# Optimization experiments

Measured on AMD Instinct MI355X. Metric: run time of the kernel, lower is better.

## Reference

```python
import jax, jax.numpy as jnp
import numpy as np

B, T, D, H, E = 2, 1024, 1024, 4096, 8


def setup_inputs() -> dict:
    key = jax.random.key(0)
    ks = jax.random.split(key, 6)
    x = jax.random.normal(ks[0], (B, T, D), dtype=jnp.float32)
    padding_mask = jnp.zeros((B, T), dtype=bool)
    # Gate: Linear(D, E, bias=False) -> weight (E, D)
    Wg = jax.random.normal(ks[1], (E, D), dtype=jnp.float32) * (1.0 / np.sqrt(D))
    # Stacked expert FFN params (torch Linear layout: weight (out, in))
    W1 = jax.random.normal(ks[2], (E, H, D), dtype=jnp.float32) * (1.0 / np.sqrt(D))
    b1 = jax.random.normal(ks[3], (E, H), dtype=jnp.float32) * 0.01
    W2 = jax.random.normal(ks[4], (E, D, H), dtype=jnp.float32) * (1.0 / np.sqrt(H))
    b2 = jax.random.normal(ks[5], (E, D), dtype=jnp.float32) * 0.01
    return {"x": x, "padding_mask": padding_mask, "Wg": Wg, "W1": W1, "b1": b1, "W2": W2, "b2": b2}


def _top2_gate(xt, pm, Wg):
    # xt: (nt, D) flattened tokens, pm: (nt,) bool padding mask
    nt, ec = xt.shape[0], Wg.shape[0]
    logits = (xt @ Wg.T).astype(jnp.float32)            # use_fp32=True
    gate_value = jax.nn.softmax(logits, axis=-1)        # (nt, E)
    gate_value = jnp.where(pm[:, None], 0.0, gate_value)
    top2_idx = jax.lax.top_k(gate_value, 2)[1]          # (nt, 2)
    keep = jax.nn.one_hot(top2_idx, ec, dtype=bool).any(axis=1)  # (nt, E) True at top1/top2
    gate_weights = jnp.where(keep, gate_value, 0.0)
    s = gate_weights.sum(axis=1, keepdims=True)
    s = jnp.where(s == 0.0, 1.0, s)
    gate_weights = gate_weights / s
    # load-balance loss: fraction of top-1 assignments vs mean gate prob per expert
    nt_real = (~pm).sum().astype(jnp.float32)
    top1_counts = (jax.nn.one_hot(top2_idx[:, 0], ec, dtype=jnp.float32)
                   * (~pm)[:, None].astype(jnp.float32)).sum(axis=0)  # (E,)
    lb_loss = ec * ((top1_counts / nt_real) * (gate_value.sum(axis=0) / nt_real)).sum()
    return lb_loss, gate_weights, gate_value


def reference(x, padding_mask, Wg, W1, b1, W2, b2):
    Bx, Tx, Dx = x.shape
    xt = x.reshape(-1, Dx)                   # (nt, D)
    pm = padding_mask.reshape(-1)            # (nt,)
    lb_loss, gw, gate_value = _top2_gate(xt, pm, Wg)
    gw = gw.astype(x.dtype)                  # (nt, E)
    # Expert FFNs (dense over experts; routing weights are zero except top-2)
    h = jax.nn.relu(jnp.einsum('nd,ehd->neh', xt, W1) + b1)   # (nt, E, H)
    y = jnp.einsum('neh,edh->ned', h, W2) + b2                # (nt, E, D)
    out = jnp.einsum('ne,ned->nd', gw, y).reshape(Bx, Tx, Dx)
    return out, gate_value, lb_loss
```

## Files before the change

### kernel.cpp

```cpp
#include <hip/hip_runtime.h>
#include <hip/hip_bf16.h>
#include <stdint.h>


#define NTOK 2048
#define DDIM 1024
#define HDIM 4096
#define NEXP 8
#define KSPLIT 2

typedef float  f32x4  __attribute__((ext_vector_type(4)));
typedef __bf16 bf16x8 __attribute__((ext_vector_type(8)));
typedef __bf16 bf16x4 __attribute__((ext_vector_type(4)));

typedef const __attribute__((address_space(1))) void g1_t;
typedef __attribute__((address_space(3))) void l3_t;
__device__ __forceinline__ void gld16(const void* g, void* l) {
  __builtin_amdgcn_global_load_lds((g1_t*)g, (l3_t*)l, 16, 0, 0);
}

__global__ void init_kernel(int* fill) {
  int t = threadIdx.x;
  if (t < NEXP) fill[t] = 0;
}

__global__ __launch_bounds__(256)
void conv_kernel(const float* __restrict__ src, __bf16* __restrict__ dst, long n8) {
  long i = (long)blockIdx.x * 256 + threadIdx.x;
  long stride = (long)gridDim.x * 256;
  for (; i < n8; i += stride) {
    f32x4 a = ((const f32x4*)src)[2 * i];
    f32x4 b = ((const f32x4*)src)[2 * i + 1];
    bf16x8 o;
#pragma unroll
    for (int q = 0; q < 4; ++q) { o[q] = (__bf16)a[q]; o[q + 4] = (__bf16)b[q]; }
    ((bf16x8*)dst)[i] = o;
  }
}

__global__ __launch_bounds__(256)
void zero_y_kernel(float* __restrict__ y) {
  size_t i = (size_t)blockIdx.x * 256 + threadIdx.x;
  ((f32x4*)y)[i] = (f32x4){0.f, 0.f, 0.f, 0.f};
}

__global__ __launch_bounds__(256)
void gate_kernel(const float* __restrict__ x, const unsigned char* __restrict__ pmask,
                 const float* __restrict__ Wg, float* __restrict__ gate_out,
                 int* __restrict__ tix, float* __restrict__ twt,
                 __bf16* __restrict__ xbf)
{
  int wave = threadIdx.x >> 6, lane = threadIdx.x & 63;
  int t = blockIdx.x * 4 + wave;
  const f32x4* x4 = (const f32x4*)(x + (size_t)t * DDIM);
  const f32x4* w4 = (const f32x4*)Wg;
  bf16x4* xb4 = (bf16x4*)(xbf + (size_t)t * DDIM);
  float acc[NEXP];
#pragma unroll
  for (int e = 0; e < NEXP; ++e) acc[e] = 0.f;
#pragma unroll
  for (int i = 0; i < 4; ++i) {
    f32x4 xv = x4[i * 64 + lane];
    bf16x4 xo;
#pragma unroll
    for (int q = 0; q < 4; ++q) xo[q] = (__bf16)xv[q];
    xb4[i * 64 + lane] = xo;
#pragma unroll
    for (int e = 0; e < NEXP; ++e) {
      f32x4 wv = w4[e * 256 + i * 64 + lane];
      acc[e] += xv[0]*wv[0] + xv[1]*wv[1] + xv[2]*wv[2] + xv[3]*wv[3];
    }
  }
#pragma unroll
  for (int e = 0; e < NEXP; ++e) {
    float v = acc[e];
#pragma unroll
    for (int off = 32; off > 0; off >>= 1) v += __shfl_xor(v, off, 64);
    acc[e] = v;
  }
  if (lane == 0) {
    bool pm = pmask[t] != 0;
    float m = acc[0];
#pragma unroll
    for (int e = 1; e < NEXP; ++e) m = fmaxf(m, acc[e]);
    float g[NEXP]; float s = 0.f;
#pragma unroll
    for (int e = 0; e < NEXP; ++e) { g[e] = expf(acc[e] - m); s += g[e]; }
    float inv = 1.f / s;
#pragma unroll
    for (int e = 0; e < NEXP; ++e) g[e] *= inv;
    if (pm) {
#pragma unroll
      for (int e = 0; e < NEXP; ++e) g[e] = 0.f;
    }
    int i1 = 0;
#pragma unroll
    for (int e = 1; e < NEXP; ++e) if (g[e] > g[i1]) i1 = e;
    int i2 = -1;
#pragma unroll
    for (int e = 0; e < NEXP; ++e) if (e != i1 && (i2 < 0 || g[e] > g[i2])) i2 = e;
    float w1 = g[i1], w2 = g[i2], ss = w1 + w2;
    if (ss == 0.f) ss = 1.f;
    w1 /= ss; w2 /= ss;
#pragma unroll
    for (int e = 0; e < NEXP; ++e) gate_out[(size_t)t * NEXP + e] = g[e];
    tix[2*t] = i1; tix[2*t+1] = i2;
    twt[2*t] = w1; twt[2*t+1] = w2;
  }
}

__global__ __launch_bounds__(1024)
void stats_kernel(const float* __restrict__ gate_out, const int* __restrict__ tix,
                  const unsigned char* __restrict__ pmask,
                  int* __restrict__ ecount, int* __restrict__ offs,
                  float* __restrict__ lb_out)
{
  int tid = threadIdx.x, lane = tid & 63, wv = tid >> 6;
  float lg[NEXP]; float lt1[NEXP]; int lec[NEXP]; float ln = 0.f;
#pragma unroll
  for (int e = 0; e < NEXP; ++e) { lg[e] = 0.f; lt1[e] = 0.f; lec[e] = 0; }
#pragma unroll
  for (int it = 0; it < NTOK / 1024; ++it) {
    int t = tid + it * 1024;
    f32x4 g0 = ((const f32x4*)(gate_out + (size_t)t * NEXP))[0];
    f32x4 g1 = ((const f32x4*)(gate_out + (size_t)t * NEXP))[1];
    lg[0] += g0[0]; lg[1] += g0[1]; lg[2] += g0[2]; lg[3] += g0[3];
    lg[4] += g1[0]; lg[5] += g1[1]; lg[6] += g1[2]; lg[7] += g1[3];
    if (!pmask[t]) {
      int i1 = tix[2*t], i2 = tix[2*t+1];
      lt1[i1] += 1.f; lec[i1] += 1; lec[i2] += 1; ln += 1.f;
    }
  }
#pragma unroll
  for (int e = 0; e < NEXP; ++e) {
#pragma unroll
    for (int off = 32; off > 0; off >>= 1) {
      lg[e]  += __shfl_xor(lg[e],  off, 64);
      lt1[e] += __shfl_xor(lt1[e], off, 64);
      lec[e] += __shfl_xor(lec[e], off, 64);
    }
  }
#pragma unroll
  for (int off = 32; off > 0; off >>= 1) ln += __shfl_xor(ln, off, 64);
  __shared__ float sg[16][NEXP], st[16][NEXP], sn[16];
  __shared__ int   se[16][NEXP];
  if (lane == 0) {
#pragma unroll
    for (int e = 0; e < NEXP; ++e) { sg[wv][e] = lg[e]; st[wv][e] = lt1[e]; se[wv][e] = lec[e]; }
    sn[wv] = ln;
  }
  __syncthreads();
  if (tid == 0) {
    float G[NEXP] = {0}, T1[NEXP] = {0}; int EC[NEXP] = {0}; float N = 0.f;
    for (int w = 0; w < 16; ++w) {
      N += sn[w];
#pragma unroll
      for (int e = 0; e < NEXP; ++e) { G[e] += sg[w][e]; T1[e] += st[w][e]; EC[e] += se[w][e]; }
    }
    int o = 0;
    for (int e = 0; e < NEXP; ++e) { ecount[e] = EC[e]; offs[e] = o; o += EC[e]; }
    if (N <= 0.f) N = 1.f;
    float lb = 0.f;
    for (int e = 0; e < NEXP; ++e) lb += (T1[e] / N) * (G[e] / N);
    lb_out[0] = (float)NEXP * lb;
  }
}

__global__ __launch_bounds__(256)
void compact_kernel(const unsigned char* __restrict__ pmask, const int* __restrict__ tix,
                    const int* __restrict__ offs, int* __restrict__ fill,
                    int* __restrict__ tok_list, int* __restrict__ slot_of)
{
  int t = blockIdx.x * 256 + threadIdx.x;
  int lane = threadIdx.x & 63;
  bool pm = pmask[t] != 0;
#pragma unroll
  for (int j = 0; j < 2; ++j) {
    int e = pm ? -1 : tix[2*t + j];
    int pos = -1;
#pragma unroll
    for (int ex = 0; ex < NEXP; ++ex) {
      unsigned long long mask = __ballot(e == ex);
      if (mask) {
        int leader = (int)(__ffsll((long long)mask) - 1);
        int base = 0;
        if (lane == leader) base = atomicAdd(&fill[ex], (int)__popcll(mask));
        base = __shfl(base, leader, 64);
        if (e == ex)
          pos = offs[ex] + base + (int)__popcll(mask & ((1ull << lane) - 1ull));
      }
    }
    if (e >= 0) { tok_list[pos] = t; slot_of[2*t + j] = pos; }
    else slot_of[2*t + j] = -1;
  }
}


__global__ __launch_bounds__(256)
void gemm1_kernel(const __bf16* __restrict__ xbf, const __bf16* __restrict__ w1bf,
                  const float* __restrict__ b1, const int* __restrict__ ecount,
                  const int* __restrict__ offs, const int* __restrict__ tok_list,
                  __bf16* __restrict__ hbuf)
{
  const int NTILE = HDIM / 128;
  const int MTILE = NTOK / 128;
  int bid = blockIdx.x;
  int e = bid / (MTILE * NTILE);
  int rem = bid % (MTILE * NTILE);
  int mt = rem / NTILE, nt = rem % NTILE;
  int cnt = ecount[e];
  if (mt * 128 >= cnt) return;
  int off = offs[e];

  __shared__ __bf16 As[2][128 * 32];
  __shared__ __bf16 Bs[2][128 * 32];

  int tid = threadIdx.x, lane = tid & 63, wave = tid >> 6;
  int wm = wave >> 1, wn = wave & 1;

  const __bf16* aP[2];
  const __bf16* bP[2];
#pragma unroll
  for (int c = 0; c < 2; ++c) {
    int row = c * 64 + (tid >> 2);
    int cd = (tid & 3) ^ ((row >> 1) & 3);
    int mrow = mt * 128 + row;
    int tok = tok_list[off + ((mrow < cnt) ? mrow : 0)];
    aP[c] = xbf + (size_t)tok * DDIM + cd * 8;
    bP[c] = w1bf + (size_t)e * HDIM * DDIM + (size_t)(nt * 128 + row) * DDIM + cd * 8;
  }
  int cg = ((lane >> 4) ^ ((lane >> 1) & 3)) << 3;

  f32x4 acc[4][4];
#pragma unroll
  for (int m = 0; m < 4; ++m)
#pragma unroll
    for (int n = 0; n < 4; ++n) acc[m][n] = (f32x4){0.f, 0.f, 0.f, 0.f};

  const int NIT = DDIM / 32;
#pragma unroll
  for (int c = 0; c < 2; ++c) {
    gld16(aP[c], &As[0][(c * 64 + wave * 16) * 32]);
    gld16(bP[c], &Bs[0][(c * 64 + wave * 16) * 32]);
  }
  __syncthreads();

  for (int it = 0; it < NIT; ++it) {
    int cur = it & 1;
    if (it + 1 < NIT) {
      int k0 = (it + 1) * 32;
#pragma unroll
      for (int c = 0; c < 2; ++c) {
        gld16(aP[c] + k0, &As[cur ^ 1][(c * 64 + wave * 16) * 32]);
        gld16(bP[c] + k0, &Bs[cur ^ 1][(c * 64 + wave * 16) * 32]);
      }
    }
    bf16x8 af[4], bfr[4];
#pragma unroll
    for (int m = 0; m < 4; ++m) af[m]  = *(const bf16x8*)&As[cur][(wm*64 + m*16 + (lane & 15)) * 32 + cg];
#pragma unroll
    for (int n = 0; n < 4; ++n) bfr[n] = *(const bf16x8*)&Bs[cur][(wn*64 + n*16 + (lane & 15)) * 32 + cg];
#pragma unroll
    for (int m = 0; m < 4; ++m)
#pragma unroll
      for (int n = 0; n < 4; ++n)
        acc[m][n] = __builtin_amdgcn_mfma_f32_16x16x32_bf16(af[m], bfr[n], acc[m][n], 0, 0, 0);
    __syncthreads();
  }

#pragma unroll
  for (int n = 0; n < 4; ++n) {
    int col = nt * 128 + wn * 64 + n * 16 + (lane & 15);
    float bias = b1[e * HDIM + col];
#pragma unroll
    for (int m = 0; m < 4; ++m) {
#pragma unroll
      for (int j = 0; j < 4; ++j) {
        int mr = mt * 128 + wm * 64 + m * 16 + ((lane >> 4) << 2) + j;
        if (mr < cnt) {
          float v = fmaxf(acc[m][n][j] + bias, 0.f);
          hbuf[(size_t)(off + mr) * HDIM + col] = (__bf16)v;
        }
      }
    }
  }
}

__global__ __launch_bounds__(256)
void gemm2_kernel(const __bf16* __restrict__ hbuf, const __bf16* __restrict__ w2bf,
                  const int* __restrict__ ecount, const int* __restrict__ offs,
                  float* __restrict__ ybuf)
{
  const int NTILE = DDIM / 128;
  const int MTILE = NTOK / 128;
  int bid = blockIdx.x;
  int e = bid / (MTILE * NTILE * KSPLIT);
  int rem = bid % (MTILE * NTILE * KSPLIT);
  int mt = rem / (NTILE * KSPLIT);
  int rem2 = rem % (NTILE * KSPLIT);
  int nt = rem2 / KSPLIT, kc = rem2 % KSPLIT;
  int cnt = ecount[e];
  if (mt * 128 >= cnt) return;
  int off = offs[e];

  __shared__ __bf16 As[2][128 * 32];
  __shared__ __bf16 Bs[2][128 * 32];

  int tid = threadIdx.x, lane = tid & 63, wave = tid >> 6;
  int wm = wave >> 1, wn = wave & 1;

  const __bf16* aP[2];
  const __bf16* bP[2];
#pragma unroll
  for (int c = 0; c < 2; ++c) {
    int row = c * 64 + (tid >> 2);
    int cd = (tid & 3) ^ ((row >> 1) & 3);
    aP[c] = hbuf + (size_t)(off + mt * 128 + row) * HDIM + cd * 8;
    bP[c] = w2bf + (size_t)e * DDIM * HDIM + (size_t)(nt * 128 + row) * HDIM + cd * 8;
  }
  int cg = ((lane >> 4) ^ ((lane >> 1) & 3)) << 3;

  f32x4 acc[4][4];
#pragma unroll
  for (int m = 0; m < 4; ++m)
#pragma unroll
    for (int n = 0; n < 4; ++n) acc[m][n] = (f32x4){0.f, 0.f, 0.f, 0.f};

  const int KCH = HDIM / KSPLIT;
  const int NIT = KCH / 32;
  int kbeg = kc * KCH;
#pragma unroll
  for (int c = 0; c < 2; ++c) {
    gld16(aP[c] + kbeg, &As[0][(c * 64 + wave * 16) * 32]);
    gld16(bP[c] + kbeg, &Bs[0][(c * 64 + wave * 16) * 32]);
  }
  __syncthreads();

  for (int it = 0; it < NIT; ++it) {
    int cur = it & 1;
    if (it + 1 < NIT) {
      int k0 = kbeg + (it + 1) * 32;
#pragma unroll
      for (int c = 0; c < 2; ++c) {
        gld16(aP[c] + k0, &As[cur ^ 1][(c * 64 + wave * 16) * 32]);
        gld16(bP[c] + k0, &Bs[cur ^ 1][(c * 64 + wave * 16) * 32]);
      }
    }
    bf16x8 af[4], bfr[4];
#pragma unroll
    for (int m = 0; m < 4; ++m) af[m]  = *(const bf16x8*)&As[cur][(wm*64 + m*16 + (lane & 15)) * 32 + cg];
#pragma unroll
    for (int n = 0; n < 4; ++n) bfr[n] = *(const bf16x8*)&Bs[cur][(wn*64 + n*16 + (lane & 15)) * 32 + cg];
#pragma unroll
    for (int m = 0; m < 4; ++m)
#pragma unroll
      for (int n = 0; n < 4; ++n)
        acc[m][n] = __builtin_amdgcn_mfma_f32_16x16x32_bf16(af[m], bfr[n], acc[m][n], 0, 0, 0);
    __syncthreads();
  }

#pragma unroll
  for (int m = 0; m < 4; ++m) {
#pragma unroll
    for (int j = 0; j < 4; ++j) {
      int mr = mt * 128 + wm * 64 + m * 16 + ((lane >> 4) << 2) + j;
      if (mr >= cnt) continue;
      int slot = off + mr;
#pragma unroll
      for (int n = 0; n < 4; ++n) {
        int col = nt * 128 + wn * 64 + n * 16 + (lane & 15);
        atomicAdd(&ybuf[(size_t)slot * DDIM + col], acc[m][n][j]);
      }
    }
  }
}

__global__ __launch_bounds__(256)
void combine_kernel(const float* __restrict__ ybuf, const int* __restrict__ slot_of,
                    const int* __restrict__ tix, const float* __restrict__ twt,
                    const float* __restrict__ b2, float* __restrict__ out)
{
  int t = blockIdx.x;
  int d4 = threadIdx.x;
  int sA = slot_of[2*t], sB = slot_of[2*t + 1];
  f32x4 r = (f32x4){0.f, 0.f, 0.f, 0.f};
  if (sA >= 0) {
    float wA = twt[2*t];
    f32x4 y = ((const f32x4*)(ybuf + (size_t)sA * DDIM))[d4];
    f32x4 b = ((const f32x4*)(b2 + (size_t)tix[2*t] * DDIM))[d4];
    r += wA * (y + b);
  }
  if (sB >= 0) {
    float wB = twt[2*t + 1];
    f32x4 y = ((const f32x4*)(ybuf + (size_t)sB * DDIM))[d4];
    f32x4 b = ((const f32x4*)(b2 + (size_t)tix[2*t + 1] * DDIM))[d4];
    r += wB * (y + b);
  }
  ((f32x4*)(out + (size_t)t * DDIM))[d4] = r;
}

extern "C" void kernel_launch(void* const* d_in, const int* in_sizes, int n_in,
                              void* d_out, int out_size, void* d_ws, size_t ws_size,
                              hipStream_t stream)
{
  const float* x  = (const float*)d_in[0];
  const unsigned char* pm = (const unsigned char*)d_in[1];
  const float* Wg = (const float*)d_in[2];
  const float* W1 = (const float*)d_in[3];
  const float* b1 = (const float*)d_in[4];
  const float* W2 = (const float*)d_in[5];
  const float* b2 = (const float*)d_in[6];
  float* out = (float*)d_out;
  float* gate_out = out + (size_t)NTOK * DDIM;
  float* lb_out = gate_out + (size_t)NTOK * NEXP;

  char* w = (char*)d_ws;
  int*   ecount   = (int*)(w + 0);
  int*   offs     = (int*)(w + 64);
  int*   fill     = (int*)(w + 128);
  int*   tix      = (int*)(w + 512);
  float* twt      = (float*)(w + 512 + 16384);
  int*   tok_list = (int*)(w + 512 + 32768);
  int*   slot_of  = (int*)(w + 512 + 49152);
  uintptr_t p = ((uintptr_t)(w + 512 + 65536) + 255) & ~(uintptr_t)255;
  __bf16* xbf  = (__bf16*)p;
  p += (size_t)NTOK * DDIM * 2;
  __bf16* wbf  = (__bf16*)p;
  p += (size_t)NEXP * HDIM * DDIM * 2;
  __bf16* hbuf = (__bf16*)p;
  p += (size_t)(2 * NTOK + 128) * HDIM * 2;
  float*  ybuf = (float*)p;

  init_kernel<<<1, 64, 0, stream>>>(fill);
  conv_kernel<<<2048, 256, 0, stream>>>(W1, wbf, (long)NEXP * HDIM * DDIM / 8);
  zero_y_kernel<<<(2 * NTOK * DDIM / 4) / 256, 256, 0, stream>>>(ybuf);
  gate_kernel<<<NTOK / 4, 256, 0, stream>>>(x, pm, Wg, gate_out, tix, twt, xbf);
  stats_kernel<<<1, 1024, 0, stream>>>(gate_out, tix, pm, ecount, offs, lb_out);
  compact_kernel<<<NTOK / 256, 256, 0, stream>>>(pm, tix, offs, fill, tok_list, slot_of);
  gemm1_kernel<<<NEXP * (NTOK / 128) * (HDIM / 128), 256, 0, stream>>>(xbf, wbf, b1, ecount, offs, tok_list, hbuf);
  conv_kernel<<<2048, 256, 0, stream>>>(W2, wbf, (long)NEXP * DDIM * HDIM / 8);
  gemm2_kernel<<<NEXP * (NTOK / 128) * (DDIM / 128) * KSPLIT, 256, 0, stream>>>(hbuf, wbf, ecount, offs, ybuf);
  combine_kernel<<<NTOK, 256, 0, stream>>>(ybuf, slot_of, tix, twt, b2, out);
}
```

Before: 267.3 us.

## Use triple-buffered LDS with prefetch distance two in both expert GEMMs

Both expert GEMM kernels go from double to triple LDS buffering and prefetch two k-steps ahead. The loop now waits on explicit vmcnt counters and a single s_barrier per iteration, replacing the two __syncthreads. This is meant to hide more global-load latency and cut one barrier per k-step. In exchange it uses 50% more LDS per block, which can lower occupancy, and it relies on hand-written waitcnt values.

```diff
diff --git a/kernel.cpp b/kernel.cpp
--- a/kernel.cpp
+++ b/kernel.cpp
@@ -212,8 +212,8 @@
   if (mt * 128 >= cnt) return;
   int off = offs[e];
 
-  __shared__ __bf16 As[2][128 * 32];
-  __shared__ __bf16 Bs[2][128 * 32];
+  __shared__ __bf16 As[3][128 * 32];
+  __shared__ __bf16 Bs[3][128 * 32];
 
   int tid = threadIdx.x, lane = tid & 63, wave = tid >> 6;
   int wm = wave >> 1, wn = wave & 1;
@@ -239,20 +239,26 @@
 
   const int NIT = DDIM / 32;
 #pragma unroll
-  for (int c = 0; c < 2; ++c) {
-    gld16(aP[c], &As[0][(c * 64 + wave * 16) * 32]);
-    gld16(bP[c], &Bs[0][(c * 64 + wave * 16) * 32]);
-  }
-  __syncthreads();
+  for (int pt = 0; pt < 2; ++pt)
+#pragma unroll
+    for (int c = 0; c < 2; ++c) {
+      gld16(aP[c] + pt * 32, &As[pt][(c * 64 + wave * 16) * 32]);
+      gld16(bP[c] + pt * 32, &Bs[pt][(c * 64 + wave * 16) * 32]);
+    }
 
   for (int it = 0; it < NIT; ++it) {
-    int cur = it & 1;
-    if (it + 1 < NIT) {
-      int k0 = (it + 1) * 32;
+    int cur = it % 3;
+    if (it + 1 < NIT) asm volatile("s_waitcnt vmcnt(4)" ::: "memory");
+    else              asm volatile("s_waitcnt vmcnt(0)" ::: "memory");
+    __builtin_amdgcn_s_barrier();
+    __builtin_amdgcn_sched_barrier(0);
+    if (it + 2 < NIT) {
+      int nb = (it + 2) % 3;
+      int k0 = (it + 2) * 32;
 #pragma unroll
       for (int c = 0; c < 2; ++c) {
-        gld16(aP[c] + k0, &As[cur ^ 1][(c * 64 + wave * 16) * 32]);
-        gld16(bP[c] + k0, &Bs[cur ^ 1][(c * 64 + wave * 16) * 32]);
+        gld16(aP[c] + k0, &As[nb][(c * 64 + wave * 16) * 32]);
+        gld16(bP[c] + k0, &Bs[nb][(c * 64 + wave * 16) * 32]);
       }
     }
     bf16x8 af[4], bfr[4];
@@ -265,7 +271,6 @@
 #pragma unroll
       for (int n = 0; n < 4; ++n)
         acc[m][n] = __builtin_amdgcn_mfma_f32_16x16x32_bf16(af[m], bfr[n], acc[m][n], 0, 0, 0);
-    __syncthreads();
   }
 
 #pragma unroll
@@ -303,8 +308,8 @@
   if (mt * 128 >= cnt) return;
   int off = offs[e];
 
-  __shared__ __bf16 As[2][128 * 32];
-  __shared__ __bf16 Bs[2][128 * 32];
+  __shared__ __bf16 As[3][128 * 32];
+  __shared__ __bf16 Bs[3][128 * 32];
 
   int tid = threadIdx.x, lane = tid & 63, wave = tid >> 6;
   int wm = wave >> 1, wn = wave & 1;
@@ -330,20 +335,26 @@
   const int NIT = KCH / 32;
   int kbeg = kc * KCH;
 #pragma unroll
-  for (int c = 0; c < 2; ++c) {
-    gld16(aP[c] + kbeg, &As[0][(c * 64 + wave * 16) * 32]);
-    gld16(bP[c] + kbeg, &Bs[0][(c * 64 + wave * 16) * 32]);
-  }
-  __syncthreads();
+  for (int pt = 0; pt < 2; ++pt)
+#pragma unroll
+    for (int c = 0; c < 2; ++c) {
+      gld16(aP[c] + kbeg + pt * 32, &As[pt][(c * 64 + wave * 16) * 32]);
+      gld16(bP[c] + kbeg + pt * 32, &Bs[pt][(c * 64 + wave * 16) * 32]);
+    }
 
   for (int it = 0; it < NIT; ++it) {
-    int cur = it & 1;
-    if (it + 1 < NIT) {
-      int k0 = kbeg + (it + 1) * 32;
+    int cur = it % 3;
+    if (it + 1 < NIT) asm volatile("s_waitcnt vmcnt(4)" ::: "memory");
+    else              asm volatile("s_waitcnt vmcnt(0)" ::: "memory");
+    __builtin_amdgcn_s_barrier();
+    __builtin_amdgcn_sched_barrier(0);
+    if (it + 2 < NIT) {
+      int nb = (it + 2) % 3;
+      int k0 = kbeg + (it + 2) * 32;
 #pragma unroll
       for (int c = 0; c < 2; ++c) {
-        gld16(aP[c] + k0, &As[cur ^ 1][(c * 64 + wave * 16) * 32]);
-        gld16(bP[c] + k0, &Bs[cur ^ 1][(c * 64 + wave * 16) * 32]);
+        gld16(aP[c] + k0, &As[nb][(c * 64 + wave * 16) * 32]);
+        gld16(bP[c] + k0, &Bs[nb][(c * 64 + wave * 16) * 32]);
       }
     }
     bf16x8 af[4], bfr[4];
@@ -356,7 +367,6 @@
 #pragma unroll
       for (int n = 0; n < 4; ++n)
         acc[m][n] = __builtin_amdgcn_mfma_f32_16x16x32_bf16(af[m], bfr[n], acc[m][n], 0, 0, 0);
-    __syncthreads();
   }
 
 #pragma unroll
```

Measured after the change: 258.8 us. 1.03x faster.

## Fuse fp32-to-bf16 weight conversion into expert GEMM B-tile loading

Applied to the files above, without the earlier changes.

Removes the two standalone passes that converted W1 and W2 from fp32 to bf16 into a workspace. The GEMM kernels now read fp32 weights straight into registers, convert them, and write swizzled bf16 tiles to shared memory, with the register stage pipelined around the MFMA loop. This saves a full read and write of 128 MB of weights in the conversion passes. In exchange, each GEMM tile reads weights at twice the byte width, the same weight tile is re-read (now as fp32) by every token tile, and the loop spends extra registers and VALU work on conversion.

```diff
diff --git a/kernel.cpp b/kernel.cpp
--- a/kernel.cpp
+++ b/kernel.cpp
@@ -22,20 +22,6 @@
 __global__ void init_kernel(int* fill) {
   int t = threadIdx.x;
   if (t < NEXP) fill[t] = 0;
-}
-
-__global__ __launch_bounds__(256)
-void conv_kernel(const float* __restrict__ src, __bf16* __restrict__ dst, long n8) {
-  long i = (long)blockIdx.x * 256 + threadIdx.x;
-  long stride = (long)gridDim.x * 256;
-  for (; i < n8; i += stride) {
-    f32x4 a = ((const f32x4*)src)[2 * i];
-    f32x4 b = ((const f32x4*)src)[2 * i + 1];
-    bf16x8 o;
-#pragma unroll
-    for (int q = 0; q < 4; ++q) { o[q] = (__bf16)a[q]; o[q + 4] = (__bf16)b[q]; }
-    ((bf16x8*)dst)[i] = o;
-  }
 }
 
 __global__ __launch_bounds__(256)
@@ -196,8 +182,21 @@
 }
 
 
-__global__ __launch_bounds__(256)
-void gemm1_kernel(const __bf16* __restrict__ xbf, const __bf16* __restrict__ w1bf,
+#define B_STAGE_LOAD(breg, bp, koff)                                   \
+  _Pragma("unroll")                                                    \
+  for (int q = 0; q < 4; ++q) breg[q] = *(const f32x4*)(bp[q] + (koff));
+
+#define B_STAGE_WRITE(dstBs, breg)                                     \
+  _Pragma("unroll")                                                    \
+  for (int q = 0; q < 4; ++q) {                                        \
+    bf16x4 o;                                                          \
+    o[0] = (__bf16)breg[q][0]; o[1] = (__bf16)breg[q][1];              \
+    o[2] = (__bf16)breg[q][2]; o[3] = (__bf16)breg[q][3];              \
+    *(bf16x4*)&(dstBs)[bwofs[q]] = o;                                  \
+  }
+
+__global__ __launch_bounds__(256)
+void gemm1_kernel(const __bf16* __restrict__ xbf, const float* __restrict__ W1,
                   const float* __restrict__ b1, const int* __restrict__ ecount,
                   const int* __restrict__ offs, const int* __restrict__ tok_list,
                   __bf16* __restrict__ hbuf)
@@ -219,7 +218,6 @@
   int wm = wave >> 1, wn = wave & 1;
 
   const __bf16* aP[2];
-  const __bf16* bP[2];
 #pragma unroll
   for (int c = 0; c < 2; ++c) {
     int row = c * 64 + (tid >> 2);
@@ -227,7 +225,15 @@
     int mrow = mt * 128 + row;
     int tok = tok_list[off + ((mrow < cnt) ? mrow : 0)];
     aP[c] = xbf + (size_t)tok * DDIM + cd * 8;
-    bP[c] = w1bf + (size_t)e * HDIM * DDIM + (size_t)(nt * 128 + row) * DDIM + cd * 8;
+  }
+  const float* bp[4];
+  int bwofs[4];
+#pragma unroll
+  for (int q = 0; q < 4; ++q) {
+    int r = (tid >> 3) + 32 * q;
+    bp[q] = W1 + (size_t)e * HDIM * DDIM + (size_t)(nt * 128 + r) * DDIM + (tid & 7) * 4;
+    int cd = (tid & 7) >> 1, h = tid & 1;
+    bwofs[q] = r * 32 + ((cd ^ ((r >> 1) & 3)) << 3) + h * 4;
   }
   int cg = ((lane >> 4) ^ ((lane >> 1) & 3)) << 3;
 
@@ -238,22 +244,20 @@
     for (int n = 0; n < 4; ++n) acc[m][n] = (f32x4){0.f, 0.f, 0.f, 0.f};
 
   const int NIT = DDIM / 32;
-#pragma unroll
-  for (int c = 0; c < 2; ++c) {
-    gld16(aP[c], &As[0][(c * 64 + wave * 16) * 32]);
-    gld16(bP[c], &Bs[0][(c * 64 + wave * 16) * 32]);
-  }
+  f32x4 breg[4];
+#pragma unroll
+  for (int c = 0; c < 2; ++c) gld16(aP[c], &As[0][(c * 64 + wave * 16) * 32]);
+  B_STAGE_LOAD(breg, bp, 0)
+  B_STAGE_WRITE(Bs[0], breg)
   __syncthreads();
 
   for (int it = 0; it < NIT; ++it) {
-    int cur = it & 1;
+    int cur = it & 1, nxt = cur ^ 1;
     if (it + 1 < NIT) {
       int k0 = (it + 1) * 32;
 #pragma unroll
-      for (int c = 0; c < 2; ++c) {
-        gld16(aP[c] + k0, &As[cur ^ 1][(c * 64 + wave * 16) * 32]);
-        gld16(bP[c] + k0, &Bs[cur ^ 1][(c * 64 + wave * 16) * 32]);
-      }
+      for (int c = 0; c < 2; ++c) gld16(aP[c] + k0, &As[nxt][(c * 64 + wave * 16) * 32]);
+      B_STAGE_LOAD(breg, bp, k0)
     }
     bf16x8 af[4], bfr[4];
 #pragma unroll
@@ -265,6 +269,7 @@
 #pragma unroll
       for (int n = 0; n < 4; ++n)
         acc[m][n] = __builtin_amdgcn_mfma_f32_16x16x32_bf16(af[m], bfr[n], acc[m][n], 0, 0, 0);
+    if (it + 1 < NIT) { B_STAGE_WRITE(Bs[nxt], breg) }
     __syncthreads();
   }
 
@@ -287,7 +292,7 @@
 }
 
 __global__ __launch_bounds__(256)
-void gemm2_kernel(const __bf16* __restrict__ hbuf, const __bf16* __restrict__ w2bf,
+void gemm2_kernel(const __bf16* __restrict__ hbuf, const float* __restrict__ W2,
                   const int* __restrict__ ecount, const int* __restrict__ offs,
                   float* __restrict__ ybuf)
 {
@@ -310,13 +315,20 @@
   int wm = wave >> 1, wn = wave & 1;
 
   const __bf16* aP[2];
-  const __bf16* bP[2];
 #pragma unroll
   for (int c = 0; c < 2; ++c) {
     int row = c * 64 + (tid >> 2);
     int cd = (tid & 3) ^ ((row >> 1) & 3);
     aP[c] = hbuf + (size_t)(off + mt * 128 + row) * HDIM + cd * 8;
-    bP[c] = w2bf + (size_t)e * DDIM * HDIM + (size_t)(nt * 128 + row) * HDIM + cd * 8;
+  }
+  const float* bp[4];
+  int bwofs[4];
+#pragma unroll
+  for (int q = 0; q < 4; ++q) {
+    int r = (tid >> 3) + 32 * q;
+    bp[q] = W2 + (size_t)e * DDIM * HDIM + (size_t)(nt * 128 + r) * HDIM + (tid & 7) * 4;
+    int cd = (tid & 7) >> 1, h = tid & 1;
+    bwofs[q] = r * 32 + ((cd ^ ((r >> 1) & 3)) << 3) + h * 4;
   }
   int cg = ((lane >> 4) ^ ((lane >> 1) & 3)) << 3;
 
@@ -329,22 +341,20 @@
   const int KCH = HDIM / KSPLIT;
   const int NIT = KCH / 32;
   int kbeg = kc * KCH;
-#pragma unroll
-  for (int c = 0; c < 2; ++c) {
-    gld16(aP[c] + kbeg, &As[0][(c * 64 + wave * 16) * 32]);
-    gld16(bP[c] + kbeg, &Bs[0][(c * 64 + wave * 16) * 32]);
-  }
+  f32x4 breg[4];
+#pragma unroll
+  for (int c = 0; c < 2; ++c) gld16(aP[c] + kbeg, &As[0][(c * 64 + wave * 16) * 32]);
+  B_STAGE_LOAD(breg, bp, kbeg)
+  B_STAGE_WRITE(Bs[0], breg)
   __syncthreads();
 
   for (int it = 0; it < NIT; ++it) {
-    int cur = it & 1;
+    int cur = it & 1, nxt = cur ^ 1;
     if (it + 1 < NIT) {
       int k0 = kbeg + (it + 1) * 32;
 #pragma unroll
-      for (int c = 0; c < 2; ++c) {
-        gld16(aP[c] + k0, &As[cur ^ 1][(c * 64 + wave * 16) * 32]);
-        gld16(bP[c] + k0, &Bs[cur ^ 1][(c * 64 + wave * 16) * 32]);
-      }
+      for (int c = 0; c < 2; ++c) gld16(aP[c] + k0, &As[nxt][(c * 64 + wave * 16) * 32]);
+      B_STAGE_LOAD(breg, bp, k0)
     }
     bf16x8 af[4], bfr[4];
 #pragma unroll
@@ -356,6 +366,7 @@
 #pragma unroll
       for (int n = 0; n < 4; ++n)
         acc[m][n] = __builtin_amdgcn_mfma_f32_16x16x32_bf16(af[m], bfr[n], acc[m][n], 0, 0, 0);
+    if (it + 1 < NIT) { B_STAGE_WRITE(Bs[nxt], breg) }
     __syncthreads();
   }
 
@@ -425,20 +436,16 @@
   uintptr_t p = ((uintptr_t)(w + 512 + 65536) + 255) & ~(uintptr_t)255;
   __bf16* xbf  = (__bf16*)p;
   p += (size_t)NTOK * DDIM * 2;
-  __bf16* wbf  = (__bf16*)p;
-  p += (size_t)NEXP * HDIM * DDIM * 2;
   __bf16* hbuf = (__bf16*)p;
   p += (size_t)(2 * NTOK + 128) * HDIM * 2;
   float*  ybuf = (float*)p;
 
   init_kernel<<<1, 64, 0, stream>>>(fill);
-  conv_kernel<<<2048, 256, 0, stream>>>(W1, wbf, (long)NEXP * HDIM * DDIM / 8);
   zero_y_kernel<<<(2 * NTOK * DDIM / 4) / 256, 256, 0, stream>>>(ybuf);
   gate_kernel<<<NTOK / 4, 256, 0, stream>>>(x, pm, Wg, gate_out, tix, twt, xbf);
   stats_kernel<<<1, 1024, 0, stream>>>(gate_out, tix, pm, ecount, offs, lb_out);
   compact_kernel<<<NTOK / 256, 256, 0, stream>>>(pm, tix, offs, fill, tok_list, slot_of);
-  gemm1_kernel<<<NEXP * (NTOK / 128) * (HDIM / 128), 256, 0, stream>>>(xbf, wbf, b1, ecount, offs, tok_list, hbuf);
-  conv_kernel<<<2048, 256, 0, stream>>>(W2, wbf, (long)NEXP * DDIM * HDIM / 8);
-  gemm2_kernel<<<NEXP * (NTOK / 128) * (DDIM / 128) * KSPLIT, 256, 0, stream>>>(hbuf, wbf, ecount, offs, ybuf);
+  gemm1_kernel<<<NEXP * (NTOK / 128) * (HDIM / 128), 256, 0, stream>>>(xbf, W1, b1, ecount, offs, tok_list, hbuf);
+  gemm2_kernel<<<NEXP * (NTOK / 128) * (DDIM / 128) * KSPLIT, 256, 0, stream>>>(hbuf, W2, ecount, offs, ybuf);
   combine_kernel<<<NTOK, 256, 0, stream>>>(ybuf, slot_of, tix, twt, b2, out);
 }
```

Result: slower. 293.5 us (+9.8%).
